# Kernel optimization log

Hardware: AMD Instinct MI355X
Metric: run time of the kernel (lower is better)

Reference implementation:

```python
import jax, jax.numpy as jnp
import numpy as np

LAMBDA_COLOR = 10.0


def _neighbors(x, p):
    """Patch-unfold: x [B,C,H,W] -> [B, P*P, C, H, W] of zero-padded shifted copies.
    Matches conv3d with diagonal one-hot [P^2,1,1,P,P] weights, padding (0,pad,pad)."""
    pad = (p - 1) // 2
    B, C, H, W = x.shape
    xp = jnp.pad(x, ((0, 0), (0, 0), (pad, pad), (pad, pad)))
    shifts = [xp[:, :, i:i + H, j:j + W] for i in range(p) for j in range(p)]
    return jnp.stack(shifts, axis=1)


def _spatial_grid(img_size):
    # np.mgrid[-1:1+eps:2/(S-1), -1:1+eps:2/(S-1)] -> [2, S, S] (y-coords, x-coords)
    lin = jnp.linspace(-1.0, 1.0, img_size, dtype=jnp.float32)
    gy, gx = jnp.meshgrid(lin, lin, indexing='ij')
    return jnp.stack([gy, gx], axis=0)[None]  # [1, 2, S, S]


def setup_inputs() -> dict:
    key = jax.random.key(0)
    k1, k2 = jax.random.split(key)
    B, S, P = 16, 256, 7
    flow = jax.random.normal(k1, (B, 2, S, S), dtype=jnp.float32)
    image = jax.random.uniform(k2, (B, 3, S, S), dtype=jnp.float32)
    return {"flow": flow, "image": image, "img_size": S, "patch_size": P}


def reference(flow, image, img_size, patch_size):
    flow = flow * img_size                                  # [B,2,H,W]
    grid = _spatial_grid(img_size)                          # [1,2,H,W]

    flow_nb = _neighbors(flow, patch_size)                  # [B,P2,2,H,W]
    img_nb = _neighbors(image, patch_size)                  # [B,P2,3,H,W]
    grid_nb = _neighbors(grid, patch_size)                  # [1,P2,2,H,W]

    im_w = jnp.sum((image[:, None] - img_nb) ** 2, axis=2)  # [B,P2,H,W]
    sp_w = jnp.sum((grid[:, None] - grid_nb) ** 2, axis=2)  # [1,P2,H,W]
    fl = jnp.sum((flow_nb - flow[:, None]) ** 2, axis=2)    # [B,P2,H,W]

    return jnp.mean(fl * jnp.exp(-(im_w * LAMBDA_COLOR + sp_w)))
```

## Files before the change

kernel.cpp:

```cpp
#include <hip/hip_runtime.h>


#define S_DIM 256
#define LOG2E 1.4426950408889634f
#define C10L2E (-14.426950408889634f)
#define N_TERMS 51380224.0f
#define FINAL_SCALE (65536.0f / N_TERMS)

typedef float v4f __attribute__((ext_vector_type(4)));
typedef int   v4i __attribute__((ext_vector_type(4)));

__device__ v4f llvm_amdgcn_raw_buffer_load_v4f32(v4i rsrc, int voffset,
                                                 int soffset, int aux)
    __asm("llvm.amdgcn.raw.buffer.load.v4f32");

__device__ inline v4i make_srd(const void* p, unsigned bytes) {
    union { v4i v; unsigned u[4]; } s;
    s.u[0] = (unsigned)(unsigned long long)p;
    s.u[1] = (unsigned)(((unsigned long long)p) >> 32);
    s.u[2] = bytes;
    s.u[3] = 0x00020000u;
    return s.v;
}

__global__ __launch_bounds__(256, 4) void flow_reg_loss_kernel(
    const float* __restrict__ flow,
    const float* __restrict__ image,
    float* __restrict__ partial)
{
    __shared__ float wave_sums[4];

    const int lane = threadIdx.x;
    const int wy   = threadIdx.y;
    const int y    = blockIdx.x * 4 + wy;
    const int b    = blockIdx.z;
    const int x0   = lane * 4;

    const v4i srdI = make_srd(image, 16u * 3u * 65536u * 4u);
    const v4i srdF = make_srd(flow,  16u * 2u * 65536u * 4u);

    const int rowx = x0 * 4 - 12;
    const int ib = b * 786432;
    const int fb = b * 524288;

    const float step = 2.0f / 255.0f;
    const float K2L2E = step * step * LOG2E;

    float acc = 0.0f;
    float ic0[4], ic1[4], ic2[4], fc0[4], fc1[4];

#define LOAD_ROW(r, yy)                                                        \
    do {                                                                       \
        const int ro = (yy) * 1024 + rowx;                                     \
        _Pragma("unroll")                                                      \
        for (int c = 0; c < 3; ++c) {                                          \
            const int v = ib + c * 262144 + ro;                                \
            const v4f a  = llvm_amdgcn_raw_buffer_load_v4f32(srdI, v, 0, 0);   \
            const v4f b4 = llvm_amdgcn_raw_buffer_load_v4f32(srdI, v, 16, 0);  \
            const v4f c4 = llvm_amdgcn_raw_buffer_load_v4f32(srdI, v, 32, 0);  \
            r[c][0] = a.x;  r[c][1] = a.y;  r[c][2]  = a.z;  r[c][3]  = a.w;   \
            r[c][4] = b4.x; r[c][5] = b4.y; r[c][6]  = b4.z; r[c][7]  = b4.w;  \
            r[c][8] = c4.x; r[c][9] = c4.y; r[c][10] = c4.z; r[c][11] = c4.w;  \
        }                                                                      \
        _Pragma("unroll")                                                      \
        for (int c = 0; c < 2; ++c) {                                          \
            const int v = fb + c * 262144 + ro;                                \
            const v4f a  = llvm_amdgcn_raw_buffer_load_v4f32(srdF, v, 0, 0);   \
            const v4f b4 = llvm_amdgcn_raw_buffer_load_v4f32(srdF, v, 16, 0);  \
            const v4f c4 = llvm_amdgcn_raw_buffer_load_v4f32(srdF, v, 32, 0);  \
            r[3+c][0] = a.x;  r[3+c][1] = a.y;  r[3+c][2]  = a.z;              \
            r[3+c][3] = a.w;  r[3+c][4] = b4.x; r[3+c][5]  = b4.y;             \
            r[3+c][6] = b4.z; r[3+c][7] = b4.w; r[3+c][8]  = c4.x;             \
            r[3+c][9] = c4.y; r[3+c][10] = c4.z; r[3+c][11] = c4.w;            \
        }                                                                      \
    } while (0)

    {
        float r[5][12];
        LOAD_ROW(r, y);
#pragma unroll
        for (int i = 0; i < 4; ++i) {
            ic0[i] = r[0][3 + i]; ic1[i] = r[1][3 + i]; ic2[i] = r[2][3 + i];
            fc0[i] = r[3][3 + i]; fc1[i] = r[4][3 + i];
        }
#pragma unroll
        for (int dx = 1; dx <= 3; ++dx) {
            const float c2 = -K2L2E * (float)(dx * dx);
#pragma unroll
            for (int i = 0; i < 4; ++i) {
                const int j = i + dx + 3;
                const float d0 = ic0[i] - r[0][j];
                const float d1 = ic1[i] - r[1][j];
                const float d2 = ic2[i] - r[2][j];
                const float imw = d0 * d0 + d1 * d1 + d2 * d2;
                const float e0 = r[3][j] - fc0[i];
                const float e1 = r[4][j] - fc1[i];
                const float fl2 = e0 * e0 + e1 * e1;
                const float w = ((unsigned)(x0 + i + dx) < S_DIM) ? 1.0f : 0.0f;
                acc += (w * fl2) * __builtin_amdgcn_exp2f(fmaf(imw, C10L2E, c2));
            }
        }
    }

#pragma unroll
    for (int dy = 1; dy <= 3; ++dy) {
        float r[5][12];
        LOAD_ROW(r, y + dy);
        const bool yin = (y + dy) < S_DIM;
#pragma unroll
        for (int dx = -3; dx <= 3; ++dx) {
            const float c2 = -K2L2E * (float)(dy * dy + dx * dx);
#pragma unroll
            for (int i = 0; i < 4; ++i) {
                const int j = i + dx + 3;
                const float d0 = ic0[i] - r[0][j];
                const float d1 = ic1[i] - r[1][j];
                const float d2 = ic2[i] - r[2][j];
                const float imw = d0 * d0 + d1 * d1 + d2 * d2;
                const float e0 = r[3][j] - fc0[i];
                const float e1 = r[4][j] - fc1[i];
                const float fl2 = e0 * e0 + e1 * e1;
                const float w = (yin && (unsigned)(x0 + i + dx) < S_DIM) ? 1.0f : 0.0f;
                acc += (w * fl2) * __builtin_amdgcn_exp2f(fmaf(imw, C10L2E, c2));
            }
        }
    }

    const int ny_in = 7 - max(0, 3 - y) - max(0, y - (S_DIM - 1 - 3));
    const float gyc = -1.0f + step * (float)y;
    float oob = 0.0f;
#pragma unroll
    for (int i = 0; i < 4; ++i) {
        const int xg = x0 + i;
        const int nx_in = 7 - max(0, 3 - xg) - max(0, xg - (S_DIM - 1 - 3));
        const float n_oob = (float)(49 - ny_in * nx_in);
        const float gxc = -1.0f + step * (float)xg;
        const float g2c = gyc * gyc + gxc * gxc;
        const float imw_c = ic0[i] * ic0[i] + ic1[i] * ic1[i] + ic2[i] * ic2[i];
        const float fl_c  = fc0[i] * fc0[i] + fc1[i] * fc1[i];
        oob += (n_oob * fl_c) *
               __builtin_amdgcn_exp2f(fmaf(imw_c, C10L2E, -g2c * LOG2E));
    }

    float acc_all = 2.0f * acc + oob;
#pragma unroll
    for (int off = 32; off > 0; off >>= 1)
        acc_all += __shfl_down(acc_all, off, 64);
    if (lane == 0) wave_sums[wy] = acc_all;
    __syncthreads();
    if (lane == 0 && wy == 0) {
        partial[blockIdx.z * gridDim.x + blockIdx.x] =
            (wave_sums[0] + wave_sums[1]) + (wave_sums[2] + wave_sums[3]);
    }
}

__global__ __launch_bounds__(256) void reduce_kernel(
    const float* __restrict__ partial, float* __restrict__ out)
{
    __shared__ float wave_sums[4];
    const int t = threadIdx.x;
    const v4f* p4 = (const v4f*)partial;
    const v4f v = p4[t];
    float s = (v.x + v.y) + (v.z + v.w);
#pragma unroll
    for (int off = 32; off > 0; off >>= 1)
        s += __shfl_down(s, off, 64);
    if ((t & 63) == 0) wave_sums[t >> 6] = s;
    __syncthreads();
    if (t == 0) {
        out[0] = ((wave_sums[0] + wave_sums[1]) + (wave_sums[2] + wave_sums[3]))
                 * FINAL_SCALE;
    }
}

extern "C" void kernel_launch(void* const* d_in, const int* in_sizes, int n_in,
                              void* d_out, int out_size, void* d_ws, size_t ws_size,
                              hipStream_t stream) {
    const float* flow  = (const float*)d_in[0];
    const float* image = (const float*)d_in[1];
    float* out = (float*)d_out;
    float* partial = (float*)d_ws;

    dim3 grid(64, 1, 16);
    dim3 block(64, 4);
    flow_reg_loss_kernel<<<grid, block, 0, stream>>>(flow, image, partial);
    reduce_kernel<<<1, 256, 0, stream>>>(partial, out);
}
```

Baseline: 84.93 us.

## Process two rows per wave to share loaded neighbor rows

Each wave now handles two adjacent output rows, so the five loaded neighbor rows serve both center rows instead of loading four rows per center row. The row loads are interleaved with computation across two register buffers, and the grid is halved with launch bounds relaxed to 2 blocks per SIMD. This cuts redundant global/L2 loads per output but raises register pressure and lowers parallelism, which could reduce occupancy and latency hiding.

```diff
diff --git a/kernel.cpp b/kernel.cpp
--- a/kernel.cpp
+++ b/kernel.cpp
@@ -23,7 +23,7 @@
     return s.v;
 }
 
-__global__ __launch_bounds__(256, 4) void flow_reg_loss_kernel(
+__global__ __launch_bounds__(256, 2) void flow_reg_loss_kernel(
     const float* __restrict__ flow,
     const float* __restrict__ image,
     float* __restrict__ partial)
@@ -31,8 +31,8 @@
     __shared__ float wave_sums[4];
 
     const int lane = threadIdx.x;
-    const int wy   = threadIdx.y;
-    const int y    = blockIdx.x * 4 + wy;
+    const int wv   = threadIdx.y;
+    const int y0   = (blockIdx.x * 4 + wv) * 2;
     const int b    = blockIdx.z;
     const int x0   = lane * 4;
 
@@ -45,9 +45,6 @@
 
     const float step = 2.0f / 255.0f;
     const float K2L2E = step * step * LOG2E;
-
-    float acc = 0.0f;
-    float ic0[4], ic1[4], ic2[4], fc0[4], fc1[4];
 
 #define LOAD_ROW(r, yy)                                                        \
     do {                                                                       \
@@ -75,80 +72,98 @@
         }                                                                      \
     } while (0)
 
-    {
-        float r[5][12];
-        LOAD_ROW(r, y);
-#pragma unroll
-        for (int i = 0; i < 4; ++i) {
-            ic0[i] = r[0][3 + i]; ic1[i] = r[1][3 + i]; ic2[i] = r[2][3 + i];
-            fc0[i] = r[3][3 + i]; fc1[i] = r[4][3 + i];
-        }
-#pragma unroll
-        for (int dx = 1; dx <= 3; ++dx) {
-            const float c2 = -K2L2E * (float)(dx * dx);
+    float A[5][12], B[5][12];
+    LOAD_ROW(A, y0);
+    LOAD_ROW(B, y0 + 1);
+
+    float ic0[2][4], ic1[2][4], ic2[2][4], fc0[2][4], fc1[2][4];
+    float acc = 0.0f;
+
+    auto tap_row = [&](int cr, const float (&r)[5][12], int dy, int dx0,
+                       bool yin) {
+#pragma unroll
+        for (int dx = dx0; dx <= 3; ++dx) {
+            const float c2 = -K2L2E * (float)(dy * dy + dx * dx);
 #pragma unroll
             for (int i = 0; i < 4; ++i) {
                 const int j = i + dx + 3;
-                const float d0 = ic0[i] - r[0][j];
-                const float d1 = ic1[i] - r[1][j];
-                const float d2 = ic2[i] - r[2][j];
+                const float d0 = ic0[cr][i] - r[0][j];
+                const float d1 = ic1[cr][i] - r[1][j];
+                const float d2 = ic2[cr][i] - r[2][j];
                 const float imw = d0 * d0 + d1 * d1 + d2 * d2;
-                const float e0 = r[3][j] - fc0[i];
-                const float e1 = r[4][j] - fc1[i];
+                const float e0 = r[3][j] - fc0[cr][i];
+                const float e1 = r[4][j] - fc1[cr][i];
                 const float fl2 = e0 * e0 + e1 * e1;
-                const float w = ((unsigned)(x0 + i + dx) < S_DIM) ? 1.0f : 0.0f;
-                acc += (w * fl2) * __builtin_amdgcn_exp2f(fmaf(imw, C10L2E, c2));
+                const float wq =
+                    (yin && (unsigned)(x0 + i + dx) < S_DIM) ? 1.0f : 0.0f;
+                acc += (wq * fl2) *
+                       __builtin_amdgcn_exp2f(fmaf(imw, C10L2E, c2));
             }
         }
-    }
-
-#pragma unroll
-    for (int dy = 1; dy <= 3; ++dy) {
-        float r[5][12];
-        LOAD_ROW(r, y + dy);
-        const bool yin = (y + dy) < S_DIM;
-#pragma unroll
-        for (int dx = -3; dx <= 3; ++dx) {
-            const float c2 = -K2L2E * (float)(dy * dy + dx * dx);
-#pragma unroll
-            for (int i = 0; i < 4; ++i) {
-                const int j = i + dx + 3;
-                const float d0 = ic0[i] - r[0][j];
-                const float d1 = ic1[i] - r[1][j];
-                const float d2 = ic2[i] - r[2][j];
-                const float imw = d0 * d0 + d1 * d1 + d2 * d2;
-                const float e0 = r[3][j] - fc0[i];
-                const float e1 = r[4][j] - fc1[i];
-                const float fl2 = e0 * e0 + e1 * e1;
-                const float w = (yin && (unsigned)(x0 + i + dx) < S_DIM) ? 1.0f : 0.0f;
-                acc += (w * fl2) * __builtin_amdgcn_exp2f(fmaf(imw, C10L2E, c2));
-            }
+    };
+
+#pragma unroll
+    for (int i = 0; i < 4; ++i) {
+        ic0[0][i] = A[0][3 + i]; ic1[0][i] = A[1][3 + i]; ic2[0][i] = A[2][3 + i];
+        fc0[0][i] = A[3][3 + i]; fc1[0][i] = A[4][3 + i];
+    }
+    tap_row(0, A, 0, 1, true);
+    LOAD_ROW(A, y0 + 2);
+
+#pragma unroll
+    for (int i = 0; i < 4; ++i) {
+        ic0[1][i] = B[0][3 + i]; ic1[1][i] = B[1][3 + i]; ic2[1][i] = B[2][3 + i];
+        fc0[1][i] = B[3][3 + i]; fc1[1][i] = B[4][3 + i];
+    }
+    tap_row(1, B, 0, 1, true);
+    tap_row(0, B, 1, -3, true);
+    LOAD_ROW(B, y0 + 3);
+
+    {
+        const bool yin = (y0 + 2) < S_DIM;
+        tap_row(0, A, 2, -3, yin);
+        tap_row(1, A, 1, -3, yin);
+    }
+    LOAD_ROW(A, y0 + 4);
+
+    {
+        const bool yin = (y0 + 3) < S_DIM;
+        tap_row(0, B, 3, -3, yin);
+        tap_row(1, B, 2, -3, yin);
+    }
+
+    tap_row(1, A, 3, -3, (y0 + 4) < S_DIM);
+
+    float oob = 0.0f;
+#pragma unroll
+    for (int cr = 0; cr < 2; ++cr) {
+        const int yg = y0 + cr;
+        const int ny_in = 7 - max(0, 3 - yg) - max(0, yg - (S_DIM - 1 - 3));
+        const float gyc = -1.0f + step * (float)yg;
+#pragma unroll
+        for (int i = 0; i < 4; ++i) {
+            const int xg = x0 + i;
+            const int nx_in = 7 - max(0, 3 - xg) - max(0, xg - (S_DIM - 1 - 3));
+            const float n_oob = (float)(49 - ny_in * nx_in);
+            const float gxc = -1.0f + step * (float)xg;
+            const float g2c = gyc * gyc + gxc * gxc;
+            const float imw_c = ic0[cr][i] * ic0[cr][i] +
+                                ic1[cr][i] * ic1[cr][i] +
+                                ic2[cr][i] * ic2[cr][i];
+            const float fl_c = fc0[cr][i] * fc0[cr][i] +
+                               fc1[cr][i] * fc1[cr][i];
+            oob += (n_oob * fl_c) *
+                   __builtin_amdgcn_exp2f(fmaf(imw_c, C10L2E, -g2c * LOG2E));
         }
-    }
-
-    const int ny_in = 7 - max(0, 3 - y) - max(0, y - (S_DIM - 1 - 3));
-    const float gyc = -1.0f + step * (float)y;
-    float oob = 0.0f;
-#pragma unroll
-    for (int i = 0; i < 4; ++i) {
-        const int xg = x0 + i;
-        const int nx_in = 7 - max(0, 3 - xg) - max(0, xg - (S_DIM - 1 - 3));
-        const float n_oob = (float)(49 - ny_in * nx_in);
-        const float gxc = -1.0f + step * (float)xg;
-        const float g2c = gyc * gyc + gxc * gxc;
-        const float imw_c = ic0[i] * ic0[i] + ic1[i] * ic1[i] + ic2[i] * ic2[i];
-        const float fl_c  = fc0[i] * fc0[i] + fc1[i] * fc1[i];
-        oob += (n_oob * fl_c) *
-               __builtin_amdgcn_exp2f(fmaf(imw_c, C10L2E, -g2c * LOG2E));
     }
 
     float acc_all = 2.0f * acc + oob;
 #pragma unroll
     for (int off = 32; off > 0; off >>= 1)
         acc_all += __shfl_down(acc_all, off, 64);
-    if (lane == 0) wave_sums[wy] = acc_all;
+    if (lane == 0) wave_sums[wv] = acc_all;
     __syncthreads();
-    if (lane == 0 && wy == 0) {
+    if (lane == 0 && wv == 0) {
         partial[blockIdx.z * gridDim.x + blockIdx.x] =
             (wave_sums[0] + wave_sums[1]) + (wave_sums[2] + wave_sums[3]);
     }
@@ -159,9 +174,9 @@
 {
     __shared__ float wave_sums[4];
     const int t = threadIdx.x;
-    const v4f* p4 = (const v4f*)partial;
-    const v4f v = p4[t];
-    float s = (v.x + v.y) + (v.z + v.w);
+    typedef float v2f __attribute__((ext_vector_type(2)));
+    const v2f v = ((const v2f*)partial)[t];
+    float s = v.x + v.y;
 #pragma unroll
     for (int off = 32; off > 0; off >>= 1)
         s += __shfl_down(s, off, 64);
@@ -181,7 +196,7 @@
     float* out = (float*)d_out;
     float* partial = (float*)d_ws;
 
-    dim3 grid(64, 1, 16);
+    dim3 grid(32, 1, 16);
     dim3 block(64, 4);
     flow_reg_loss_kernel<<<grid, block, 0, stream>>>(flow, image, partial);
     reduce_kernel<<<1, 256, 0, stream>>>(partial, out);
```

Result: no change. 83.35 us (-1.9%).
